# Optimization experiments

Measured on AMD Instinct MI355X. Metric: run time of the kernel, lower is better.

Reference implementation:

```python
import jax, jax.numpy as jnp
import numpy as np

N = 100000   # nodes
E = 1600000  # edges (before self-loops)
D = 64       # feature/hidden dim


def setup_inputs() -> dict:
    key = jax.random.key(0)
    ks = jax.random.split(key, 12)
    x = jax.random.normal(ks[0], (N, D), dtype=jnp.float32)
    edge_index = jax.random.randint(ks[1], (2, E), 0, N, dtype=jnp.int32)
    params = {}
    for i in range(4):
        params[f"W{i}"] = jax.random.normal(ks[2 + 2 * i], (D, D), dtype=jnp.float32) * (1.0 / np.sqrt(D))
        params[f"b{i}"] = jnp.zeros((D,), dtype=jnp.float32)
    params["Wfc"] = jax.random.normal(ks[10], (D, 1), dtype=jnp.float32) * (1.0 / np.sqrt(D))
    params["bfc"] = jnp.zeros((1,), dtype=jnp.float32)
    return {"x": x, "edge_index": edge_index, **params}


def _gcn_norm(edge_index, n):
    # add self-loops, compute symmetric normalization coefficients
    loop = jnp.arange(n, dtype=edge_index.dtype)
    row = jnp.concatenate([edge_index[0], loop])  # source
    col = jnp.concatenate([edge_index[1], loop])  # target
    deg = jax.ops.segment_sum(jnp.ones_like(col, dtype=jnp.float32), col, num_segments=n)
    dinv = jnp.where(deg > 0, 1.0 / jnp.sqrt(deg), 0.0)
    norm = dinv[row] * dinv[col]  # [E+N]
    return row, col, norm


def _gcn_conv(x, row, col, norm, W, b, n):
    xw = x @ W                              # [N, D] small GEMM
    msgs = xw[row] * norm[:, None]          # gather + scale, [E+N, D]
    out = jax.ops.segment_sum(msgs, col, num_segments=n)  # scatter-add
    return out + b


def reference(x, edge_index, W0, b0, W1, b1, W2, b2, W3, b3, Wfc, bfc):
    row, col, norm = _gcn_norm(edge_index, N)
    h = x
    for W, b in ((W0, b0), (W1, b1), (W2, b2), (W3, b3)):
        h = jax.nn.relu(_gcn_conv(h, row, col, norm, W, b, N))
    return (h @ Wfc + bfc).squeeze(-1)  # [N]
```

## Files before the change

kernel.cpp:

```cpp
#include <hip/hip_runtime.h>
#include <hip/hip_fp16.h>
#include <math.h>

#define D 64
#define CAP 56
#define BSH 5
#define BW_ (1 << BSH)
#define BCAP 768
#define NBLKA 256

__global__ void k_binA(const int* __restrict__ rows, const int* __restrict__ cols,
                       int* __restrict__ bcnt, unsigned int* __restrict__ bbuf,
                       int e, int nb) {
    __shared__ int hist[4096];
    int tid = threadIdx.x;
    int chunk = (e + gridDim.x - 1) / gridDim.x;
    int lo = blockIdx.x * chunk;
    int hi = min(lo + chunk, e);
    for (int k = tid; k < nb; k += blockDim.x) hist[k] = 0;
    __syncthreads();
    for (int i = lo + tid; i < hi; i += blockDim.x)
        atomicAdd(&hist[cols[i] >> BSH], 1);
    __syncthreads();
    for (int k = tid; k < nb; k += blockDim.x) {
        int h = hist[k];
        hist[k] = (h > 0) ? atomicAdd(&bcnt[k], h) : 0;
    }
    __syncthreads();
    for (int i = lo + tid; i < hi; i += blockDim.x) {
        int c = cols[i];
        int b = c >> BSH;
        int p = atomicAdd(&hist[b], 1);
        if (p < BCAP)
            bbuf[(size_t)b * BCAP + p] = ((unsigned)rows[i] << BSH) | (unsigned)(c & (BW_ - 1));
    }
}

__global__ void k_binB(const int* __restrict__ bcnt, const unsigned int* __restrict__ bbuf,
                       int* __restrict__ cnt, float* __restrict__ dinv,
                       int* __restrict__ srows, int n) {
    __shared__ int c32[BW_];
    int b = blockIdx.x;
    int tid = threadIdx.x;
    if (tid < BW_) c32[tid] = 0;
    __syncthreads();
    int cbase = b << BSH;
    int mE = bcnt[b];
    if (mE > BCAP) mE = BCAP;
    for (int i = tid; i < mE; i += blockDim.x) {
        unsigned pk = bbuf[(size_t)b * BCAP + i];
        int node = pk & (BW_ - 1);
        int row = (int)(pk >> BSH);
        int p = atomicAdd(&c32[node], 1);
        if (p < CAP) srows[(size_t)(cbase + node) * CAP + p] = row;
    }
    __syncthreads();
    if (tid < BW_ && cbase + tid < n) {
        int m = c32[tid];
        cnt[cbase + tid] = m;
        dinv[cbase + tid] = 1.0f / sqrtf((float)(m + 1));
    }
}

__global__ void k_prescale(const float* __restrict__ x, const float* __restrict__ dinv,
                           uint2* __restrict__ xp, int n) {
    int t = blockIdx.x * blockDim.x + threadIdx.x;
    if (t >= n * (D / 4)) return;
    float di = dinv[t >> 4];
    float4 v = ((const float4*)x)[t];
    __half2 h0 = __float22half2_rn(make_float2(v.x * di, v.y * di));
    __half2 h1 = __float22half2_rn(make_float2(v.z * di, v.w * di));
    uint2 st;
    st.x = *(unsigned*)&h0;
    st.y = *(unsigned*)&h1;
    xp[t] = st;
}

template <bool LAST>
__global__ void k_layer4(const int* __restrict__ cnt, const int* __restrict__ srows,
                         const uint2* __restrict__ hp, const float* __restrict__ dinv,
                         const float4* __restrict__ W4, const float4* __restrict__ b4,
                         const float4* __restrict__ Wfc4, const float* __restrict__ bfc,
                         uint2* __restrict__ hpout, float* __restrict__ out, int n) {
    int wave = (blockIdx.x * blockDim.x + threadIdx.x) >> 6;
    int lane = threadIdx.x & 63;
    int sub   = lane & 15;
    int qbase = lane & 48;
    int c = wave * 4 + (lane >> 4);
    bool valid = (c < n);
    int cc = valid ? c : 0;

    int m = valid ? cnt[cc] : 0;
    m = (m > CAP) ? CAP : m;

    const int* seg = srows + (size_t)cc * CAP;
    int idx[4];
    idx[0] = seg[sub];
    idx[1] = seg[sub + 16];
    idx[2] = seg[sub + 32];
    idx[3] = (sub < CAP - 48) ? seg[sub + 48] : 0;

    float4 v;
    {
        uint2 sf = hp[(size_t)cc * 16 + sub];
        float2 f0 = __half22float2(*(__half2*)&sf.x);
        float2 f1 = __half22float2(*(__half2*)&sf.y);
        v.x = f0.x; v.y = f0.y; v.z = f1.x; v.w = f1.y;
    }

#pragma unroll
    for (int i0 = 0; i0 < CAP; i0 += 8) {
        if (i0 < m) {
            uint2 a[8];
#pragma unroll
            for (int j = 0; j < 8; ++j) {
                int i = i0 + j;
                int r = __shfl(idx[i >> 4], qbase + (i & 15), 64);
                r = (i < m) ? r : cc;
                a[j] = hp[(size_t)r * 16 + sub];
            }
#pragma unroll
            for (int j = 0; j < 8; ++j) {
                if (i0 + j < m) {
                    float2 f0 = __half22float2(*(__half2*)&a[j].x);
                    float2 f1 = __half22float2(*(__half2*)&a[j].y);
                    v.x += f0.x; v.y += f0.y; v.z += f1.x; v.w += f1.y;
                }
            }
        }
    }

    float di = dinv[cc];
    float4 t;
    t.x = v.x * di; t.y = v.y * di; t.z = v.z * di; t.w = v.w * di;

    float4 s = b4[sub];
#pragma unroll
    for (int p = 0; p < 16; ++p) {
        float tw0 = __shfl(t.x, qbase + p, 64);
        float tw1 = __shfl(t.y, qbase + p, 64);
        float tw2 = __shfl(t.z, qbase + p, 64);
        float tw3 = __shfl(t.w, qbase + p, 64);
        float4 w0 = W4[(size_t)(4 * p + 0) * 16 + sub];
        float4 w1 = W4[(size_t)(4 * p + 1) * 16 + sub];
        float4 w2 = W4[(size_t)(4 * p + 2) * 16 + sub];
        float4 w3 = W4[(size_t)(4 * p + 3) * 16 + sub];
        s.x = fmaf(tw0, w0.x, s.x); s.y = fmaf(tw0, w0.y, s.y);
        s.z = fmaf(tw0, w0.z, s.z); s.w = fmaf(tw0, w0.w, s.w);
        s.x = fmaf(tw1, w1.x, s.x); s.y = fmaf(tw1, w1.y, s.y);
        s.z = fmaf(tw1, w1.z, s.z); s.w = fmaf(tw1, w1.w, s.w);
        s.x = fmaf(tw2, w2.x, s.x); s.y = fmaf(tw2, w2.y, s.y);
        s.z = fmaf(tw2, w2.z, s.z); s.w = fmaf(tw2, w2.w, s.w);
        s.x = fmaf(tw3, w3.x, s.x); s.y = fmaf(tw3, w3.y, s.y);
        s.z = fmaf(tw3, w3.z, s.z); s.w = fmaf(tw3, w3.w, s.w);
    }
    float4 hv;
    hv.x = fmaxf(s.x, 0.0f); hv.y = fmaxf(s.y, 0.0f);
    hv.z = fmaxf(s.z, 0.0f); hv.w = fmaxf(s.w, 0.0f);

    if (!LAST) {
        if (valid) {
            __half2 h0 = __float22half2_rn(make_float2(hv.x * di, hv.y * di));
            __half2 h1 = __float22half2_rn(make_float2(hv.z * di, hv.w * di));
            uint2 st;
            st.x = *(unsigned*)&h0;
            st.y = *(unsigned*)&h1;
            hpout[(size_t)cc * 16 + sub] = st;
        }
    } else {
        float4 wf = Wfc4[sub];
        float u = hv.x * wf.x + hv.y * wf.y + hv.z * wf.z + hv.w * wf.w;
        u += __shfl_xor(u, 1, 64);
        u += __shfl_xor(u, 2, 64);
        u += __shfl_xor(u, 4, 64);
        u += __shfl_xor(u, 8, 64);
        if (valid && sub == 0) out[cc] = u + bfc[0];
    }
}

extern "C" void kernel_launch(void* const* d_in, const int* in_sizes, int n_in,
                              void* d_out, int out_size, void* d_ws, size_t ws_size,
                              hipStream_t stream) {
    const float* x  = (const float*)d_in[0];
    const int*   ei = (const int*)d_in[1];
    const int n = in_sizes[0] / D;
    const int e = in_sizes[1] / 2;
    const int* rows = ei;
    const int* cols = ei + e;
    const float* W[4] = {(const float*)d_in[2], (const float*)d_in[4],
                         (const float*)d_in[6], (const float*)d_in[8]};
    const float* b[4] = {(const float*)d_in[3], (const float*)d_in[5],
                         (const float*)d_in[7], (const float*)d_in[9]};
    const float* Wfc = (const float*)d_in[10];
    const float* bfc = (const float*)d_in[11];
    float* out = (float*)d_out;

    size_t na = ((size_t)n + 255) & ~(size_t)255;
    int*   cnt   = (int*)d_ws;
    float* dinv  = (float*)(cnt + na);
    int*   srows = (int*)(dinv + na);
    size_t nseg  = (((size_t)n * CAP) + 255) & ~(size_t)255;
    uint2* bufA  = (uint2*)(srows + nseg);
    uint2* bufB  = bufA + (size_t)n * 16;

    const int nb = (n + BW_ - 1) >> BSH;
    int*          bcnt = (int*)bufA;
    unsigned int* bbuf = (unsigned int*)bufB;

    const int B = 256;
    const int layer_grid = ((size_t)n * 16 + B - 1) / B;

    hipMemsetAsync(bcnt, 0, (size_t)nb * sizeof(int), stream);
    k_binA<<<NBLKA, B, 0, stream>>>(rows, cols, bcnt, bbuf, e, nb);
    k_binB<<<nb, B, 0, stream>>>(bcnt, bbuf, cnt, dinv, srows, n);
    k_prescale<<<((size_t)n * (D / 4) + B - 1) / B, B, 0, stream>>>(x, dinv, bufA, n);

    k_layer4<false><<<layer_grid, B, 0, stream>>>(cnt, srows, bufA, dinv,
                                                  (const float4*)W[0], (const float4*)b[0],
                                                  nullptr, nullptr, bufB, nullptr, n);
    k_layer4<false><<<layer_grid, B, 0, stream>>>(cnt, srows, bufB, dinv,
                                                  (const float4*)W[1], (const float4*)b[1],
                                                  nullptr, nullptr, bufA, nullptr, n);
    k_layer4<false><<<layer_grid, B, 0, stream>>>(cnt, srows, bufA, dinv,
                                                  (const float4*)W[2], (const float4*)b[2],
                                                  nullptr, nullptr, bufB, nullptr, n);
    k_layer4<true><<<layer_grid, B, 0, stream>>>(cnt, srows, bufB, dinv,
                                                 (const float4*)W[3], (const float4*)b[3],
                                                 (const float4*)Wfc, bfc, nullptr, out, n);
}
```

Baseline: 353.0 us.

## Process eight nodes per wave with 16-byte fp16 row gathers

Remaps the per-layer aggregation kernel so each wave handles 8 nodes with 8 lanes per node. Each lane now gathers a 16-byte chunk (8 halves) of a neighbour row instead of 8 bytes, which halves the number of load instructions per edge and doubles nodes per wave. The dense 64x64 transform is rewritten to match, with each lane producing 8 outputs and issuing more weight loads and shuffles. Register pressure rises with 7 index registers and 8-wide accumulators, which could lower occupancy.

Result: faster. 328.6 us (-6.9%).

```diff
diff --git a/kernel.cpp b/kernel.cpp
--- a/kernel.cpp
+++ b/kernel.cpp
@@ -77,16 +77,16 @@
 }
 
 template <bool LAST>
-__global__ void k_layer4(const int* __restrict__ cnt, const int* __restrict__ srows,
-                         const uint2* __restrict__ hp, const float* __restrict__ dinv,
+__global__ void k_layer8(const int* __restrict__ cnt, const int* __restrict__ srows,
+                         const uint4* __restrict__ hp, const float* __restrict__ dinv,
                          const float4* __restrict__ W4, const float4* __restrict__ b4,
                          const float4* __restrict__ Wfc4, const float* __restrict__ bfc,
-                         uint2* __restrict__ hpout, float* __restrict__ out, int n) {
-    int wave = (blockIdx.x * blockDim.x + threadIdx.x) >> 6;
-    int lane = threadIdx.x & 63;
-    int sub   = lane & 15;
-    int qbase = lane & 48;
-    int c = wave * 4 + (lane >> 4);
+                         uint4* __restrict__ hpout, float* __restrict__ out, int n) {
+    int wave  = (blockIdx.x * blockDim.x + threadIdx.x) >> 6;
+    int lane  = threadIdx.x & 63;
+    int sub   = lane & 7;
+    int gbase = lane & 56;
+    int c = wave * 8 + (lane >> 3);
     bool valid = (c < n);
     int cc = valid ? c : 0;
 
@@ -94,86 +94,94 @@
     m = (m > CAP) ? CAP : m;
 
     const int* seg = srows + (size_t)cc * CAP;
-    int idx[4];
-    idx[0] = seg[sub];
-    idx[1] = seg[sub + 16];
-    idx[2] = seg[sub + 32];
-    idx[3] = (sub < CAP - 48) ? seg[sub + 48] : 0;
-
-    float4 v;
+    int idx[7];
+#pragma unroll
+    for (int r = 0; r < 7; ++r) idx[r] = seg[sub + 8 * r];
+
+    float v[8];
     {
-        uint2 sf = hp[(size_t)cc * 16 + sub];
-        float2 f0 = __half22float2(*(__half2*)&sf.x);
-        float2 f1 = __half22float2(*(__half2*)&sf.y);
-        v.x = f0.x; v.y = f0.y; v.z = f1.x; v.w = f1.y;
-    }
-
-#pragma unroll
-    for (int i0 = 0; i0 < CAP; i0 += 8) {
-        if (i0 < m) {
-            uint2 a[8];
-#pragma unroll
-            for (int j = 0; j < 8; ++j) {
-                int i = i0 + j;
-                int r = __shfl(idx[i >> 4], qbase + (i & 15), 64);
-                r = (i < m) ? r : cc;
-                a[j] = hp[(size_t)r * 16 + sub];
+        uint4 sr = hp[(size_t)cc * 8 + sub];
+        float2 f0 = __half22float2(*(__half2*)&sr.x);
+        float2 f1 = __half22float2(*(__half2*)&sr.y);
+        float2 f2 = __half22float2(*(__half2*)&sr.z);
+        float2 f3 = __half22float2(*(__half2*)&sr.w);
+        v[0] = f0.x; v[1] = f0.y; v[2] = f1.x; v[3] = f1.y;
+        v[4] = f2.x; v[5] = f2.y; v[6] = f3.x; v[7] = f3.y;
+    }
+
+#pragma unroll
+    for (int j = 0; j < 7; ++j) {
+        if (8 * j < m) {
+            uint4 a[8];
+#pragma unroll
+            for (int u = 0; u < 8; ++u) {
+                int s = 8 * j + u;
+                int r = __shfl(idx[j], gbase + u, 64);
+                uint4 av = make_uint4(0u, 0u, 0u, 0u);
+                if (s < m)
+                    av = hp[(size_t)r * 8 + sub];
+                a[u] = av;
             }
 #pragma unroll
-            for (int j = 0; j < 8; ++j) {
-                if (i0 + j < m) {
-                    float2 f0 = __half22float2(*(__half2*)&a[j].x);
-                    float2 f1 = __half22float2(*(__half2*)&a[j].y);
-                    v.x += f0.x; v.y += f0.y; v.z += f1.x; v.w += f1.y;
-                }
+            for (int u = 0; u < 8; ++u) {
+                float2 f0 = __half22float2(*(__half2*)&a[u].x);
+                float2 f1 = __half22float2(*(__half2*)&a[u].y);
+                float2 f2 = __half22float2(*(__half2*)&a[u].z);
+                float2 f3 = __half22float2(*(__half2*)&a[u].w);
+                v[0] += f0.x; v[1] += f0.y; v[2] += f1.x; v[3] += f1.y;
+                v[4] += f2.x; v[5] += f2.y; v[6] += f3.x; v[7] += f3.y;
             }
         }
     }
 
     float di = dinv[cc];
-    float4 t;
-    t.x = v.x * di; t.y = v.y * di; t.z = v.z * di; t.w = v.w * di;
-
-    float4 s = b4[sub];
-#pragma unroll
-    for (int p = 0; p < 16; ++p) {
-        float tw0 = __shfl(t.x, qbase + p, 64);
-        float tw1 = __shfl(t.y, qbase + p, 64);
-        float tw2 = __shfl(t.z, qbase + p, 64);
-        float tw3 = __shfl(t.w, qbase + p, 64);
-        float4 w0 = W4[(size_t)(4 * p + 0) * 16 + sub];
-        float4 w1 = W4[(size_t)(4 * p + 1) * 16 + sub];
-        float4 w2 = W4[(size_t)(4 * p + 2) * 16 + sub];
-        float4 w3 = W4[(size_t)(4 * p + 3) * 16 + sub];
-        s.x = fmaf(tw0, w0.x, s.x); s.y = fmaf(tw0, w0.y, s.y);
-        s.z = fmaf(tw0, w0.z, s.z); s.w = fmaf(tw0, w0.w, s.w);
-        s.x = fmaf(tw1, w1.x, s.x); s.y = fmaf(tw1, w1.y, s.y);
-        s.z = fmaf(tw1, w1.z, s.z); s.w = fmaf(tw1, w1.w, s.w);
-        s.x = fmaf(tw2, w2.x, s.x); s.y = fmaf(tw2, w2.y, s.y);
-        s.z = fmaf(tw2, w2.z, s.z); s.w = fmaf(tw2, w2.w, s.w);
-        s.x = fmaf(tw3, w3.x, s.x); s.y = fmaf(tw3, w3.y, s.y);
-        s.z = fmaf(tw3, w3.z, s.z); s.w = fmaf(tw3, w3.w, s.w);
-    }
-    float4 hv;
-    hv.x = fmaxf(s.x, 0.0f); hv.y = fmaxf(s.y, 0.0f);
-    hv.z = fmaxf(s.z, 0.0f); hv.w = fmaxf(s.w, 0.0f);
+    float t[8];
+#pragma unroll
+    for (int i = 0; i < 8; ++i) t[i] = v[i] * di;
+
+    float s8[8];
+    {
+        float4 bb0 = b4[2 * sub];
+        float4 bb1 = b4[2 * sub + 1];
+        s8[0] = bb0.x; s8[1] = bb0.y; s8[2] = bb0.z; s8[3] = bb0.w;
+        s8[4] = bb1.x; s8[5] = bb1.y; s8[6] = bb1.z; s8[7] = bb1.w;
+    }
+#pragma unroll
+    for (int q = 0; q < 8; ++q) {
+#pragma unroll
+        for (int u = 0; u < 8; ++u) {
+            float tw = __shfl(t[u], gbase + q, 64);
+            float4 w0 = W4[(size_t)(8 * q + u) * 16 + 2 * sub];
+            float4 w1 = W4[(size_t)(8 * q + u) * 16 + 2 * sub + 1];
+            s8[0] = fmaf(tw, w0.x, s8[0]); s8[1] = fmaf(tw, w0.y, s8[1]);
+            s8[2] = fmaf(tw, w0.z, s8[2]); s8[3] = fmaf(tw, w0.w, s8[3]);
+            s8[4] = fmaf(tw, w1.x, s8[4]); s8[5] = fmaf(tw, w1.y, s8[5]);
+            s8[6] = fmaf(tw, w1.z, s8[6]); s8[7] = fmaf(tw, w1.w, s8[7]);
+        }
+    }
+    float hv[8];
+#pragma unroll
+    for (int i = 0; i < 8; ++i) hv[i] = fmaxf(s8[i], 0.0f);
 
     if (!LAST) {
         if (valid) {
-            __half2 h0 = __float22half2_rn(make_float2(hv.x * di, hv.y * di));
-            __half2 h1 = __float22half2_rn(make_float2(hv.z * di, hv.w * di));
-            uint2 st;
-            st.x = *(unsigned*)&h0;
-            st.y = *(unsigned*)&h1;
-            hpout[(size_t)cc * 16 + sub] = st;
+            __half2 h0 = __float22half2_rn(make_float2(hv[0] * di, hv[1] * di));
+            __half2 h1 = __float22half2_rn(make_float2(hv[2] * di, hv[3] * di));
+            __half2 h2 = __float22half2_rn(make_float2(hv[4] * di, hv[5] * di));
+            __half2 h3 = __float22half2_rn(make_float2(hv[6] * di, hv[7] * di));
+            uint4 st;
+            st.x = *(unsigned*)&h0; st.y = *(unsigned*)&h1;
+            st.z = *(unsigned*)&h2; st.w = *(unsigned*)&h3;
+            hpout[(size_t)cc * 8 + sub] = st;
         }
     } else {
-        float4 wf = Wfc4[sub];
-        float u = hv.x * wf.x + hv.y * wf.y + hv.z * wf.z + hv.w * wf.w;
+        float4 wf0 = Wfc4[2 * sub];
+        float4 wf1 = Wfc4[2 * sub + 1];
+        float u = hv[0] * wf0.x + hv[1] * wf0.y + hv[2] * wf0.z + hv[3] * wf0.w
+                + hv[4] * wf1.x + hv[5] * wf1.y + hv[6] * wf1.z + hv[7] * wf1.w;
         u += __shfl_xor(u, 1, 64);
         u += __shfl_xor(u, 2, 64);
         u += __shfl_xor(u, 4, 64);
-        u += __shfl_xor(u, 8, 64);
         if (valid && sub == 0) out[cc] = u + bfc[0];
     }
 }
@@ -200,31 +208,31 @@
     float* dinv  = (float*)(cnt + na);
     int*   srows = (int*)(dinv + na);
     size_t nseg  = (((size_t)n * CAP) + 255) & ~(size_t)255;
-    uint2* bufA  = (uint2*)(srows + nseg);
-    uint2* bufB  = bufA + (size_t)n * 16;
+    uint4* bufA  = (uint4*)(srows + nseg);
+    uint4* bufB  = bufA + (size_t)n * 8;
 
     const int nb = (n + BW_ - 1) >> BSH;
     int*          bcnt = (int*)bufA;
     unsigned int* bbuf = (unsigned int*)bufB;
 
     const int B = 256;
-    const int layer_grid = ((size_t)n * 16 + B - 1) / B;
+    const int layer_grid = (int)(((size_t)(n + 7) / 8 * 64 + B - 1) / B);
 
     hipMemsetAsync(bcnt, 0, (size_t)nb * sizeof(int), stream);
     k_binA<<<NBLKA, B, 0, stream>>>(rows, cols, bcnt, bbuf, e, nb);
     k_binB<<<nb, B, 0, stream>>>(bcnt, bbuf, cnt, dinv, srows, n);
-    k_prescale<<<((size_t)n * (D / 4) + B - 1) / B, B, 0, stream>>>(x, dinv, bufA, n);
-
-    k_layer4<false><<<layer_grid, B, 0, stream>>>(cnt, srows, bufA, dinv,
+    k_prescale<<<((size_t)n * (D / 4) + B - 1) / B, B, 0, stream>>>(x, dinv, (uint2*)bufA, n);
+
+    k_layer8<false><<<layer_grid, B, 0, stream>>>(cnt, srows, bufA, dinv,
                                                   (const float4*)W[0], (const float4*)b[0],
                                                   nullptr, nullptr, bufB, nullptr, n);
-    k_layer4<false><<<layer_grid, B, 0, stream>>>(cnt, srows, bufB, dinv,
+    k_layer8<false><<<layer_grid, B, 0, stream>>>(cnt, srows, bufB, dinv,
                                                   (const float4*)W[1], (const float4*)b[1],
                                                   nullptr, nullptr, bufA, nullptr, n);
-    k_layer4<false><<<layer_grid, B, 0, stream>>>(cnt, srows, bufA, dinv,
+    k_layer8<false><<<layer_grid, B, 0, stream>>>(cnt, srows, bufA, dinv,
                                                   (const float4*)W[2], (const float4*)b[2],
                                                   nullptr, nullptr, bufB, nullptr, n);
-    k_layer4<true><<<layer_grid, B, 0, stream>>>(cnt, srows, bufB, dinv,
+    k_layer8<true><<<layer_grid, B, 0, stream>>>(cnt, srows, bufB, dinv,
                                                  (const float4*)W[3], (const float4*)b[3],
                                                  (const float4*)Wfc, bfc, nullptr, out, n);
 }
```
